# Performance work log

Measured on AMD Instinct MI355X. Metric: run time of the kernel, lower is better.

## Reference

```python
import jax, jax.numpy as jnp
import numpy as np

B, K, C, O = 8, 100000, 16, 16
HG, WG = 512, 512
ALPHA_PRIOR = 1.0
KERN = np.array([[0.075, 0.125, 0.075], [0.125, 0.3, 0.125], [0.075, 0.125, 0.075]], dtype=np.float32)


def setup_inputs() -> dict:
    key = jax.random.key(0)
    k1, k2, k3, k4, k5 = jax.random.split(key, 5)
    node_feat = jax.random.normal(k1, (B, K, C), dtype=jnp.float32)
    node_xy = jax.random.uniform(k2, (B, K, 2), dtype=jnp.float32, minval=0.0, maxval=WG - 1.0)
    node_types = jax.random.randint(k3, (B, K), 0, 2)
    # kaiming_normal_ fan_out: std = sqrt(2 / fan_out), fan_out = O*1*1
    std = (2.0 / O) ** 0.5
    w_obj = jax.random.normal(k4, (O, C), dtype=jnp.float32) * std
    w_prior = jax.random.normal(k5, (O, C), dtype=jnp.float32) * std
    hw = np.array([HG, WG], dtype=np.int64)
    return {"node_feat": node_feat, "node_xy": node_xy, "hw": hw,
            "node_types": node_types, "w_obj": w_obj, "w_prior": w_prior}


def rasterize(node_feat, node_xy, weight, H, W):
    # node_feat [B,K,C], node_xy [B,K,2], weight [B,K] 0/1 mask (masked scatter == scatter of zeros)
    xs = jnp.clip(jnp.round(node_xy[..., 0]), 0, W - 1).astype(jnp.int32)
    ys = jnp.clip(jnp.round(node_xy[..., 1]), 0, H - 1).astype(jnp.int32)
    idx = ys * W + xs  # [B,K] flat grid index
    src = node_feat * weight[..., None]  # zero out non-selected nodes

    def scat(idx_b, src_b):
        return jnp.zeros((H * W, src_b.shape[-1]), src_b.dtype).at[idx_b].add(src_b)

    grid = jax.vmap(scat)(idx, src)  # [B,HW,C]
    return grid.reshape(grid.shape[0], H, W, -1).transpose(0, 3, 1, 2)  # [B,C,H,W]


def splat3x3(x, kern):
    # depthwise 3x3 conv, groups = C
    c = x.shape[1]
    w = jnp.broadcast_to(kern[None, None], (c, 1, 3, 3))
    return jax.lax.conv_general_dilated(
        x, w, window_strides=(1, 1), padding='SAME',
        dimension_numbers=('NCHW', 'OIHW', 'NCHW'), feature_group_count=c)


def reference(node_feat, node_xy, hw, node_types, w_obj, w_prior):
    H, W = int(hw[0]), int(hw[1])
    kern = jnp.asarray(KERN)
    mask_obj = (node_types == 0).astype(node_feat.dtype)
    mask_prior = (node_types == 1).astype(node_feat.dtype)
    map_obj = splat3x3(rasterize(node_feat, node_xy, mask_obj, H, W), kern)
    map_prior = splat3x3(rasterize(node_feat, node_xy, mask_prior, H, W), kern)
    # rasterize + splat run under torch.no_grad() in the original
    map_obj = jax.lax.stop_gradient(map_obj)
    map_prior = jax.lax.stop_gradient(map_prior)
    out = jnp.einsum('oc,bchw->bohw', w_obj, map_obj) \
        + ALPHA_PRIOR * jnp.einsum('oc,bchw->bohw', w_prior, map_prior)
    return out
```

## Files before the change

kernel.cpp:

```cpp
#include <hip/hip_runtime.h>

#define B_ 8
#define K_ 100000
#define NODES (B_ * K_)
#define C_ 16
#define O_ 16
#define H_ 512
#define W_ 512
#define TSX 32
#define TSY 16
#define NTX (W_ / TSX)
#define NTY (H_ / TSY)
#define NBKT (B_ * NTX * NTY)
#define CAP 512
#define EX (TSX + 2)
#define EY (TSY + 2)
#define PLANE (EX * EY)
#define FB 1000
#define FPB (FB / B_)
#define FCHUNK (K_ / FPB)
#define IDS_OFF 16384
#define P_OFF (IDS_OFF + NBKT * CAP * 4)
#define WS_NEED ((size_t)P_OFF + (size_t)NODES * O_ * 4)

__device__ __forceinline__ float bf_lo(unsigned int u) {
    union { unsigned int i; float f; } v; v.i = u << 16; return v.f;
}
__device__ __forceinline__ float bf_hi(unsigned int u) {
    union { unsigned int i; float f; } v; v.i = u & 0xffff0000u; return v.f;
}
__device__ __forceinline__ unsigned short f2bf(float f) {
    union { float f; unsigned int u; } v; v.f = f;
    unsigned int u = v.u;
    u += 0x7fffu + ((u >> 16) & 1u);
    return (unsigned short)(u >> 16);
}

__device__ __forceinline__ int probe_fp32_ballot(const unsigned int* xy) {
    const int lane = threadIdx.x & 63;
    int bad = 0;
    #pragma unroll
    for (int k = 0; k < 4; ++k) {
        float lo = bf_lo(xy[lane + (k << 6)]);
        bad |= !(lo >= 0.0f && lo <= 512.0f);
    }
    return __ballot(bad) != 0ull;
}

__device__ __forceinline__ void decode_xy(const void* xy, int fp32, int n,
                                          int& xs, int& ys)
{
    float x, y;
    if (fp32) { float2 p = ((const float2*)xy)[n]; x = p.x; y = p.y; }
    else { unsigned int u = ((const unsigned int*)xy)[n]; x = bf_lo(u); y = bf_hi(u); }
    xs = min(max((int)rintf(x), 0), W_ - 1);
    ys = min(max((int)rintf(y), 0), H_ - 1);
}

template<bool PRE>
__global__ __launch_bounds__(256) void fill_bins(
    const void* __restrict__ feat, const void* __restrict__ xy,
    const int* __restrict__ types,
    const void* __restrict__ w_obj, const void* __restrict__ w_prior,
    int* __restrict__ cursor, int* __restrict__ ids, float* __restrict__ p)
{
    __shared__ int hist[NTX * NTY];
    __shared__ unsigned int rec[FCHUNK];
    __shared__ float wl[PRE ? 2 * O_ * C_ : 2];

    const int tid = threadIdx.x;
    const int fp32 = probe_fp32_ballot((const unsigned int*)xy);
    for (int j = tid; j < NTX * NTY; j += 256) hist[j] = 0;
    if constexpr (PRE) {
        for (int i = tid; i < 2 * O_ * C_; i += 256) {
            if (fp32) {
                wl[i] = (i < O_ * C_) ? ((const float*)w_obj)[i]
                                      : ((const float*)w_prior)[i - O_ * C_];
            } else {
                unsigned short raw = (i < O_ * C_)
                    ? ((const unsigned short*)w_obj)[i]
                    : ((const unsigned short*)w_prior)[i - O_ * C_];
                union { unsigned int u; float f; } v; v.u = ((unsigned int)raw) << 16;
                wl[i] = v.f;
            }
        }
    }
    __syncthreads();

    const int bb = blockIdx.x / FPB;
    const int local0 = (blockIdx.x % FPB) * FCHUNK;
    const int s = bb * K_ + local0;

    for (int ii = tid; ii < FCHUNK; ii += 256) {
        const int n = s + ii;
        int xs, ys; decode_xy(xy, fp32, n, xs, ys);
        const int t = (types[n] != 0);
        rec[ii] = (unsigned)(xs | (ys << 9) | (t << 18));

        if constexpr (PRE) {
            float f[16];
            if (fp32) {
                const float4* ff = (const float4*)feat + (size_t)n * 4;
                float4 a = ff[0], b2 = ff[1], c = ff[2], d = ff[3];
                f[0]=a.x; f[1]=a.y; f[2]=a.z; f[3]=a.w;
                f[4]=b2.x; f[5]=b2.y; f[6]=b2.z; f[7]=b2.w;
                f[8]=c.x; f[9]=c.y; f[10]=c.z; f[11]=c.w;
                f[12]=d.x; f[13]=d.y; f[14]=d.z; f[15]=d.w;
            } else {
                const uint4* ff = (const uint4*)feat + (size_t)n * 2;
                uint4 A = ff[0], Bv = ff[1];
                f[0]=bf_lo(A.x);  f[1]=bf_hi(A.x);  f[2]=bf_lo(A.y);  f[3]=bf_hi(A.y);
                f[4]=bf_lo(A.z);  f[5]=bf_hi(A.z);  f[6]=bf_lo(A.w);  f[7]=bf_hi(A.w);
                f[8]=bf_lo(Bv.x); f[9]=bf_hi(Bv.x); f[10]=bf_lo(Bv.y); f[11]=bf_hi(Bv.y);
                f[12]=bf_lo(Bv.z); f[13]=bf_hi(Bv.z); f[14]=bf_lo(Bv.w); f[15]=bf_hi(Bv.w);
            }
            const float* wrow = &wl[t * O_ * C_];
            float pv[16];
            #pragma unroll
            for (int o = 0; o < O_; ++o) {
                float acc = 0.f;
                #pragma unroll
                for (int c = 0; c < C_; ++c) acc = fmaf(wrow[o * C_ + c], f[c], acc);
                pv[o] = acc;
            }
            float4* pout = (float4*)(p + (size_t)n * O_);
            pout[0] = make_float4(pv[0],  pv[1],  pv[2],  pv[3]);
            pout[1] = make_float4(pv[4],  pv[5],  pv[6],  pv[7]);
            pout[2] = make_float4(pv[8],  pv[9],  pv[10], pv[11]);
            pout[3] = make_float4(pv[12], pv[13], pv[14], pv[15]);
        }

        int xlo = max((xs - 1) >> 5, 0), xhi = min((xs + 1) >> 5, NTX - 1);
        int ylo = max((ys - 1) >> 4, 0), yhi = min((ys + 1) >> 4, NTY - 1);
        for (int tyy = ylo; tyy <= yhi; ++tyy)
            for (int txx = xlo; txx <= xhi; ++txx)
                atomicAdd(&hist[tyy * NTX + txx], 1);
    }
    __syncthreads();

    for (int j = tid; j < NTX * NTY; j += 256) {
        int c = hist[j];
        hist[j] = c ? atomicAdd(&cursor[bb * NTX * NTY + j], c) : 0;
    }
    __syncthreads();

    for (int ii = tid; ii < FCHUNK; ii += 256) {
        unsigned r = rec[ii];
        int xs = r & 511, ys = (r >> 9) & 511, t = (r >> 18) & 1;
        int local = local0 + ii;
        int xlo = max((xs - 1) >> 5, 0), xhi = min((xs + 1) >> 5, NTX - 1);
        int ylo = max((ys - 1) >> 4, 0), yhi = min((ys + 1) >> 4, NTY - 1);
        for (int tyy = ylo; tyy <= yhi; ++tyy)
            for (int txx = xlo; txx <= xhi; ++txx) {
                int bk = tyy * NTX + txx;
                int slot = atomicAdd(&hist[bk], 1);
                if (slot < CAP) {
                    int lx = xs - (txx << 5) + 1;
                    int ly = ys - (tyy << 4) + 1;
                    ids[(bb * NTX * NTY + bk) * CAP + slot] =
                        local | (t << 17) | (lx << 18) | (ly << 24);
                }
            }
    }
}

template<bool PRE>
__global__ __launch_bounds__(512) void tile_fused(
    const void* __restrict__ src ,
    const void* __restrict__ xy,
    const void* __restrict__ w_obj, const void* __restrict__ w_prior,
    const int* __restrict__ cursor, const int* __restrict__ ids,
    void* __restrict__ out)
{
    __shared__ float accs[O_ * PLANE];
    __shared__ float wl[PRE ? 2 : 2 * O_ * C_];

    const int tid = threadIdx.x;
    const int tx = blockIdx.x, ty = blockIdx.y, b = blockIdx.z;
    const int bucket = (b * NTY + ty) * NTX + tx;
    int cnt = cursor[bucket];
    if (cnt > CAP) cnt = CAP;
    const int fp32 = probe_fp32_ballot((const unsigned int*)xy);

    float f[16];
    int t = 0, lx = 0, ly = 0;
    const bool active = (tid < cnt);
    if (active) {
        const unsigned pck = (unsigned)ids[bucket * CAP + tid];
        const int local = pck & 0x1FFFF;
        t  = (pck >> 17) & 1;
        lx = (pck >> 18) & 63;
        ly = (pck >> 24) & 31;
        const size_t n = (size_t)b * K_ + local;
        if constexpr (PRE) {
            const float4* pp = (const float4*)src + n * 4;
            float4 a = pp[0], b2 = pp[1], c = pp[2], d = pp[3];
            f[0]=a.x; f[1]=a.y; f[2]=a.z; f[3]=a.w;
            f[4]=b2.x; f[5]=b2.y; f[6]=b2.z; f[7]=b2.w;
            f[8]=c.x; f[9]=c.y; f[10]=c.z; f[11]=c.w;
            f[12]=d.x; f[13]=d.y; f[14]=d.z; f[15]=d.w;
        } else {
            if (fp32) {
                const float4* ff = (const float4*)src + n * 4;
                float4 a = ff[0], b2 = ff[1], c = ff[2], d = ff[3];
                f[0]=a.x; f[1]=a.y; f[2]=a.z; f[3]=a.w;
                f[4]=b2.x; f[5]=b2.y; f[6]=b2.z; f[7]=b2.w;
                f[8]=c.x; f[9]=c.y; f[10]=c.z; f[11]=c.w;
                f[12]=d.x; f[13]=d.y; f[14]=d.z; f[15]=d.w;
            } else {
                const uint4* ff = (const uint4*)src + n * 2;
                uint4 A = ff[0], Bv = ff[1];
                f[0]=bf_lo(A.x);  f[1]=bf_hi(A.x);  f[2]=bf_lo(A.y);  f[3]=bf_hi(A.y);
                f[4]=bf_lo(A.z);  f[5]=bf_hi(A.z);  f[6]=bf_lo(A.w);  f[7]=bf_hi(A.w);
                f[8]=bf_lo(Bv.x); f[9]=bf_hi(Bv.x); f[10]=bf_lo(Bv.y); f[11]=bf_hi(Bv.y);
                f[12]=bf_lo(Bv.z); f[13]=bf_hi(Bv.z); f[14]=bf_lo(Bv.w); f[15]=bf_hi(Bv.w);
            }
        }
    }

    for (int i = tid; i < O_ * PLANE; i += 512) accs[i] = 0.f;
    if constexpr (!PRE) {
        if (fp32) {
            for (int i = tid; i < 2 * O_ * C_; i += 512)
                wl[i] = (i < O_ * C_) ? ((const float*)w_obj)[i]
                                      : ((const float*)w_prior)[i - O_ * C_];
        } else {
            for (int i = tid; i < 2 * O_ * C_; i += 512) {
                unsigned short raw = (i < O_ * C_)
                    ? ((const unsigned short*)w_obj)[i]
                    : ((const unsigned short*)w_prior)[i - O_ * C_];
                union { unsigned int u; float f; } v; v.u = ((unsigned int)raw) << 16;
                wl[i] = v.f;
            }
        }
    }
    __syncthreads();

    if (active) {
        float* cell = &accs[ly * EX + lx];
        if constexpr (PRE) {
            #pragma unroll
            for (int o = 0; o < O_; ++o) atomicAdd(cell + o * PLANE, f[o]);
        } else {
            const float* wrow = &wl[t * O_ * C_];
            #pragma unroll
            for (int o = 0; o < O_; ++o) {
                float acc = 0.f;
                #pragma unroll
                for (int c = 0; c < C_; ++c) acc = fmaf(wrow[o * C_ + c], f[c], acc);
                atomicAdd(cell + o * PLANE, acc);
            }
        }
    }
    __syncthreads();

    const int x = tid & 31;
    const int o = tid >> 5;
    const float* pl = &accs[o * PLANE + x];
    float hA2 = 0.f, hA1 = 0.f, hB1 = 0.f;
    const int x0 = tx * TSX, y0 = ty * TSY;
    const size_t obase = (((size_t)(b * O_ + o)) * H_) * W_;

    #pragma unroll
    for (int iy = 0; iy < EY; ++iy) {
        float l = pl[iy * EX], c = pl[iy * EX + 1], r = pl[iy * EX + 2];
        float sfx = l + r;
        float hA = fmaf(0.075f, sfx, 0.125f * c);
        float hB = fmaf(0.125f, sfx, 0.3f * c);
        if (iy >= 2) {
            float v = hA2 + hB1 + hA;
            size_t oi = obase + (size_t)(y0 + iy - 2) * W_ + (x0 + x);
            if (fp32) __builtin_nontemporal_store(v, (float*)out + oi);
            else      __builtin_nontemporal_store(f2bf(v), (unsigned short*)out + oi);
        }
        hA2 = hA1; hA1 = hA; hB1 = hB;
    }
}

extern "C" void kernel_launch(void* const* d_in, const int* in_sizes, int n_in,
                              void* d_out, int out_size, void* d_ws, size_t ws_size,
                              hipStream_t stream)
{
    const void* feat = d_in[0];
    const void* xy = d_in[1];
    const int* types = (const int*)d_in[3];
    const void* w_obj = d_in[4];
    const void* w_prior = d_in[5];

    int* cursor = (int*)d_ws;
    int* ids = (int*)((char*)d_ws + IDS_OFF);
    float* p = (float*)((char*)d_ws + P_OFF);

    hipMemsetAsync(cursor, 0, NBKT * sizeof(int), stream);
    if (ws_size >= WS_NEED) {
        fill_bins<true><<<FB, 256, 0, stream>>>(feat, xy, types, w_obj, w_prior,
                                                cursor, ids, p);
        tile_fused<true><<<dim3(NTX, NTY, B_), 512, 0, stream>>>(
            p, xy, w_obj, w_prior, cursor, ids, d_out);
    } else {
        fill_bins<false><<<FB, 256, 0, stream>>>(feat, xy, types, w_obj, w_prior,
                                                 cursor, ids, p);
        tile_fused<false><<<dim3(NTX, NTY, B_), 512, 0, stream>>>(
            feat, xy, w_obj, w_prior, cursor, ids, d_out);
    }
}
```

Before: 285.3 us.

## Scatter projected node values directly into per-tile slots instead of index lists

Adds a new path where the fill kernel projects each node's features through the weights and writes the 16 projected values plus packed local coordinates straight into per-bucket slot storage, using global atomic cursors. The tile kernel then reads these values contiguously instead of gathering through node ids into a separate projected buffer. This removes the random indirect gather in the tile stage, at the cost of writing projected data up to four times for nodes near tile edges and needing a larger workspace. The fill grid also doubles in block count, and global atomics replace shared histograms.

```diff
diff --git a/kernel.cpp b/kernel.cpp
--- a/kernel.cpp
+++ b/kernel.cpp
@@ -16,12 +16,21 @@
 #define EX (TSX + 2)
 #define EY (TSY + 2)
 #define PLANE (EX * EY)
+
 #define FB 1000
 #define FPB (FB / B_)
 #define FCHUNK (K_ / FPB)
 #define IDS_OFF 16384
 #define P_OFF (IDS_OFF + NBKT * CAP * 4)
-#define WS_NEED ((size_t)P_OFF + (size_t)NODES * O_ * 4)
+#define WS_NEED_PRE ((size_t)P_OFF + (size_t)NODES * O_ * 4)
+
+#define SFB 2000
+#define SFPB (SFB / B_)
+#define SFCHUNK (K_ / SFPB)
+#define LXY_OFF 16384
+static inline size_t ws_need_scat(int scap) {
+    return (size_t)LXY_OFF + (size_t)NBKT * scap * 2 + (size_t)NBKT * scap * 64;
+}
 
 __device__ __forceinline__ float bf_lo(unsigned int u) {
     union { unsigned int i; float f; } v; v.i = u << 16; return v.f;
@@ -57,6 +66,164 @@
     ys = min(max((int)rintf(y), 0), H_ - 1);
 }
 
+__device__ __forceinline__ void load_feat16(const void* feat, size_t n, int fp32,
+                                            float* f)
+{
+    if (fp32) {
+        const float4* ff = (const float4*)feat + n * 4;
+        float4 a = ff[0], b2 = ff[1], c = ff[2], d = ff[3];
+        f[0]=a.x; f[1]=a.y; f[2]=a.z; f[3]=a.w;
+        f[4]=b2.x; f[5]=b2.y; f[6]=b2.z; f[7]=b2.w;
+        f[8]=c.x; f[9]=c.y; f[10]=c.z; f[11]=c.w;
+        f[12]=d.x; f[13]=d.y; f[14]=d.z; f[15]=d.w;
+    } else {
+        const uint4* ff = (const uint4*)feat + n * 2;
+        uint4 A = ff[0], Bv = ff[1];
+        f[0]=bf_lo(A.x);  f[1]=bf_hi(A.x);  f[2]=bf_lo(A.y);  f[3]=bf_hi(A.y);
+        f[4]=bf_lo(A.z);  f[5]=bf_hi(A.z);  f[6]=bf_lo(A.w);  f[7]=bf_hi(A.w);
+        f[8]=bf_lo(Bv.x); f[9]=bf_hi(Bv.x); f[10]=bf_lo(Bv.y); f[11]=bf_hi(Bv.y);
+        f[12]=bf_lo(Bv.z); f[13]=bf_hi(Bv.z); f[14]=bf_lo(Bv.w); f[15]=bf_hi(Bv.w);
+    }
+}
+
+__device__ __forceinline__ void load_weights_lds(float* wl, int fp32,
+                                                 const void* w_obj,
+                                                 const void* w_prior,
+                                                 int tid, int nthreads)
+{
+    for (int i = tid; i < 2 * O_ * C_; i += nthreads) {
+        if (fp32) {
+            wl[i] = (i < O_ * C_) ? ((const float*)w_obj)[i]
+                                  : ((const float*)w_prior)[i - O_ * C_];
+        } else {
+            unsigned short raw = (i < O_ * C_)
+                ? ((const unsigned short*)w_obj)[i]
+                : ((const unsigned short*)w_prior)[i - O_ * C_];
+            union { unsigned int u; float f; } v; v.u = ((unsigned int)raw) << 16;
+            wl[i] = v.f;
+        }
+    }
+}
+
+__global__ __launch_bounds__(256) void fill_scat(
+    const void* __restrict__ feat, const void* __restrict__ xy,
+    const int* __restrict__ types,
+    const void* __restrict__ w_obj, const void* __restrict__ w_prior,
+    int* __restrict__ cursor, float* __restrict__ slots,
+    unsigned short* __restrict__ lxy, int scap)
+{
+    __shared__ float wl[2 * O_ * C_];
+
+    const int tid = threadIdx.x;
+    const int fp32 = probe_fp32_ballot((const unsigned int*)xy);
+    load_weights_lds(wl, fp32, w_obj, w_prior, tid, 256);
+    __syncthreads();
+
+    const int bb = blockIdx.x / SFPB;
+    const int local0 = (blockIdx.x % SFPB) * SFCHUNK;
+    const int s = bb * K_ + local0;
+
+    for (int ii = tid; ii < SFCHUNK; ii += 256) {
+        const int n = s + ii;
+        int xs, ys; decode_xy(xy, fp32, n, xs, ys);
+        const int t = (types[n] != 0);
+
+        float f[16];
+        load_feat16(feat, (size_t)n, fp32, f);
+        const float* wrow = &wl[t * O_ * C_];
+        float pv[16];
+        #pragma unroll
+        for (int o = 0; o < O_; ++o) {
+            float acc = 0.f;
+            #pragma unroll
+            for (int c = 0; c < C_; ++c) acc = fmaf(wrow[o * C_ + c], f[c], acc);
+            pv[o] = acc;
+        }
+
+        const int xlo = max((xs - 1) >> 5, 0), xhi = min((xs + 1) >> 5, NTX - 1);
+        const int ylo = max((ys - 1) >> 4, 0), yhi = min((ys + 1) >> 4, NTY - 1);
+        for (int tyy = ylo; tyy <= yhi; ++tyy)
+            for (int txx = xlo; txx <= xhi; ++txx) {
+                const int bkg = (bb * NTY + tyy) * NTX + txx;
+                const int slot = atomicAdd(&cursor[bkg], 1);
+                if (slot < scap) {
+                    const size_t base = (size_t)bkg * scap + slot;
+                    float4* sp = (float4*)(slots + base * 16);
+                    sp[0] = make_float4(pv[0],  pv[1],  pv[2],  pv[3]);
+                    sp[1] = make_float4(pv[4],  pv[5],  pv[6],  pv[7]);
+                    sp[2] = make_float4(pv[8],  pv[9],  pv[10], pv[11]);
+                    sp[3] = make_float4(pv[12], pv[13], pv[14], pv[15]);
+                    const int lx = xs - (txx << 5) + 1;
+                    const int ly = ys - (tyy << 4) + 1;
+                    lxy[base] = (unsigned short)(lx | (ly << 8));
+                }
+            }
+    }
+}
+
+__global__ __launch_bounds__(512) void tile_scat(
+    const float* __restrict__ slots, const unsigned short* __restrict__ lxy,
+    const void* __restrict__ xy,
+    const int* __restrict__ cursor, void* __restrict__ out, int scap)
+{
+    __shared__ float accs[O_ * PLANE];
+
+    const int tid = threadIdx.x;
+    const int tx = blockIdx.x, ty = blockIdx.y, b = blockIdx.z;
+    const int bucket = (b * NTY + ty) * NTX + tx;
+    int cnt = cursor[bucket];
+    if (cnt > scap) cnt = scap;
+    const int fp32 = probe_fp32_ballot((const unsigned int*)xy);
+
+    float f[16];
+    int lx = 0, ly = 0;
+    const bool active = (tid < cnt);
+    if (active) {
+        const size_t base = (size_t)bucket * scap + tid;
+        const unsigned short lv = lxy[base];
+        lx = lv & 63;
+        ly = (lv >> 8) & 31;
+        const float4* sp = (const float4*)(slots + base * 16);
+        float4 a = sp[0], b2 = sp[1], c = sp[2], d = sp[3];
+        f[0]=a.x; f[1]=a.y; f[2]=a.z; f[3]=a.w;
+        f[4]=b2.x; f[5]=b2.y; f[6]=b2.z; f[7]=b2.w;
+        f[8]=c.x; f[9]=c.y; f[10]=c.z; f[11]=c.w;
+        f[12]=d.x; f[13]=d.y; f[14]=d.z; f[15]=d.w;
+    }
+
+    for (int i = tid; i < O_ * PLANE; i += 512) accs[i] = 0.f;
+    __syncthreads();
+
+    if (active) {
+        float* cell = &accs[ly * EX + lx];
+        #pragma unroll
+        for (int o = 0; o < O_; ++o) atomicAdd(cell + o * PLANE, f[o]);
+    }
+    __syncthreads();
+
+    const int x = tid & 31;
+    const int o = tid >> 5;
+    const float* pl = &accs[o * PLANE + x];
+    float hA2 = 0.f, hA1 = 0.f, hB1 = 0.f;
+    const int x0 = tx * TSX, y0 = ty * TSY;
+    const size_t obase = (((size_t)(b * O_ + o)) * H_) * W_;
+
+    #pragma unroll
+    for (int iy = 0; iy < EY; ++iy) {
+        float l = pl[iy * EX], c = pl[iy * EX + 1], r = pl[iy * EX + 2];
+        float sfx = l + r;
+        float hA = fmaf(0.075f, sfx, 0.125f * c);
+        float hB = fmaf(0.125f, sfx, 0.3f * c);
+        if (iy >= 2) {
+            float v = hA2 + hB1 + hA;
+            size_t oi = obase + (size_t)(y0 + iy - 2) * W_ + (x0 + x);
+            if (fp32) __builtin_nontemporal_store(v, (float*)out + oi);
+            else      __builtin_nontemporal_store(f2bf(v), (unsigned short*)out + oi);
+        }
+        hA2 = hA1; hA1 = hA; hB1 = hB;
+    }
+}
+
 template<bool PRE>
 __global__ __launch_bounds__(256) void fill_bins(
     const void* __restrict__ feat, const void* __restrict__ xy,
@@ -71,20 +238,7 @@
     const int tid = threadIdx.x;
     const int fp32 = probe_fp32_ballot((const unsigned int*)xy);
     for (int j = tid; j < NTX * NTY; j += 256) hist[j] = 0;
-    if constexpr (PRE) {
-        for (int i = tid; i < 2 * O_ * C_; i += 256) {
-            if (fp32) {
-                wl[i] = (i < O_ * C_) ? ((const float*)w_obj)[i]
-                                      : ((const float*)w_prior)[i - O_ * C_];
-            } else {
-                unsigned short raw = (i < O_ * C_)
-                    ? ((const unsigned short*)w_obj)[i]
-                    : ((const unsigned short*)w_prior)[i - O_ * C_];
-                union { unsigned int u; float f; } v; v.u = ((unsigned int)raw) << 16;
-                wl[i] = v.f;
-            }
-        }
-    }
+    if constexpr (PRE) load_weights_lds(wl, fp32, w_obj, w_prior, tid, 256);
     __syncthreads();
 
     const int bb = blockIdx.x / FPB;
@@ -99,21 +253,7 @@
 
         if constexpr (PRE) {
             float f[16];
-            if (fp32) {
-                const float4* ff = (const float4*)feat + (size_t)n * 4;
-                float4 a = ff[0], b2 = ff[1], c = ff[2], d = ff[3];
-                f[0]=a.x; f[1]=a.y; f[2]=a.z; f[3]=a.w;
-                f[4]=b2.x; f[5]=b2.y; f[6]=b2.z; f[7]=b2.w;
-                f[8]=c.x; f[9]=c.y; f[10]=c.z; f[11]=c.w;
-                f[12]=d.x; f[13]=d.y; f[14]=d.z; f[15]=d.w;
-            } else {
-                const uint4* ff = (const uint4*)feat + (size_t)n * 2;
-                uint4 A = ff[0], Bv = ff[1];
-                f[0]=bf_lo(A.x);  f[1]=bf_hi(A.x);  f[2]=bf_lo(A.y);  f[3]=bf_hi(A.y);
-                f[4]=bf_lo(A.z);  f[5]=bf_hi(A.z);  f[6]=bf_lo(A.w);  f[7]=bf_hi(A.w);
-                f[8]=bf_lo(Bv.x); f[9]=bf_hi(Bv.x); f[10]=bf_lo(Bv.y); f[11]=bf_hi(Bv.y);
-                f[12]=bf_lo(Bv.z); f[13]=bf_hi(Bv.z); f[14]=bf_lo(Bv.w); f[15]=bf_hi(Bv.w);
-            }
+            load_feat16(feat, (size_t)n, fp32, f);
             const float* wrow = &wl[t * O_ * C_];
             float pv[16];
             #pragma unroll
@@ -166,8 +306,7 @@
 
 template<bool PRE>
 __global__ __launch_bounds__(512) void tile_fused(
-    const void* __restrict__ src ,
-    const void* __restrict__ xy,
+    const void* __restrict__ src, const void* __restrict__ xy,
     const void* __restrict__ w_obj, const void* __restrict__ w_prior,
     const int* __restrict__ cursor, const int* __restrict__ ids,
     void* __restrict__ out)
@@ -200,40 +339,12 @@
             f[8]=c.x; f[9]=c.y; f[10]=c.z; f[11]=c.w;
             f[12]=d.x; f[13]=d.y; f[14]=d.z; f[15]=d.w;
         } else {
-            if (fp32) {
-                const float4* ff = (const float4*)src + n * 4;
-                float4 a = ff[0], b2 = ff[1], c = ff[2], d = ff[3];
-                f[0]=a.x; f[1]=a.y; f[2]=a.z; f[3]=a.w;
-                f[4]=b2.x; f[5]=b2.y; f[6]=b2.z; f[7]=b2.w;
-                f[8]=c.x; f[9]=c.y; f[10]=c.z; f[11]=c.w;
-                f[12]=d.x; f[13]=d.y; f[14]=d.z; f[15]=d.w;
-            } else {
-                const uint4* ff = (const uint4*)src + n * 2;
-                uint4 A = ff[0], Bv = ff[1];
-                f[0]=bf_lo(A.x);  f[1]=bf_hi(A.x);  f[2]=bf_lo(A.y);  f[3]=bf_hi(A.y);
-                f[4]=bf_lo(A.z);  f[5]=bf_hi(A.z);  f[6]=bf_lo(A.w);  f[7]=bf_hi(A.w);
-                f[8]=bf_lo(Bv.x); f[9]=bf_hi(Bv.x); f[10]=bf_lo(Bv.y); f[11]=bf_hi(Bv.y);
-                f[12]=bf_lo(Bv.z); f[13]=bf_hi(Bv.z); f[14]=bf_lo(Bv.w); f[15]=bf_hi(Bv.w);
-            }
+            load_feat16(src, n, fp32, f);
         }
     }
 
     for (int i = tid; i < O_ * PLANE; i += 512) accs[i] = 0.f;
-    if constexpr (!PRE) {
-        if (fp32) {
-            for (int i = tid; i < 2 * O_ * C_; i += 512)
-                wl[i] = (i < O_ * C_) ? ((const float*)w_obj)[i]
-                                      : ((const float*)w_prior)[i - O_ * C_];
-        } else {
-            for (int i = tid; i < 2 * O_ * C_; i += 512) {
-                unsigned short raw = (i < O_ * C_)
-                    ? ((const unsigned short*)w_obj)[i]
-                    : ((const unsigned short*)w_prior)[i - O_ * C_];
-                union { unsigned int u; float f; } v; v.u = ((unsigned int)raw) << 16;
-                wl[i] = v.f;
-            }
-        }
-    }
+    if constexpr (!PRE) load_weights_lds(wl, fp32, w_obj, w_prior, tid, 512);
     __syncthreads();
 
     if (active) {
@@ -288,16 +399,29 @@
     const void* w_prior = d_in[5];
 
     int* cursor = (int*)d_ws;
-    int* ids = (int*)((char*)d_ws + IDS_OFF);
-    float* p = (float*)((char*)d_ws + P_OFF);
-
     hipMemsetAsync(cursor, 0, NBKT * sizeof(int), stream);
-    if (ws_size >= WS_NEED) {
+
+    int scap = 0;
+    if (ws_size >= ws_need_scat(512)) scap = 512;
+    else if (ws_size >= ws_need_scat(384)) scap = 384;
+
+    if (scap) {
+        unsigned short* lxy = (unsigned short*)((char*)d_ws + LXY_OFF);
+        float* slots = (float*)((char*)d_ws + LXY_OFF + (size_t)NBKT * scap * 2);
+        fill_scat<<<SFB, 256, 0, stream>>>(feat, xy, types, w_obj, w_prior,
+                                           cursor, slots, lxy, scap);
+        tile_scat<<<dim3(NTX, NTY, B_), 512, 0, stream>>>(
+            slots, lxy, xy, cursor, d_out, scap);
+    } else if (ws_size >= WS_NEED_PRE) {
+        int* ids = (int*)((char*)d_ws + IDS_OFF);
+        float* p = (float*)((char*)d_ws + P_OFF);
         fill_bins<true><<<FB, 256, 0, stream>>>(feat, xy, types, w_obj, w_prior,
                                                 cursor, ids, p);
         tile_fused<true><<<dim3(NTX, NTY, B_), 512, 0, stream>>>(
             p, xy, w_obj, w_prior, cursor, ids, d_out);
     } else {
+        int* ids = (int*)((char*)d_ws + IDS_OFF);
+        float* p = (float*)((char*)d_ws + P_OFF);
         fill_bins<false><<<FB, 256, 0, stream>>>(feat, xy, types, w_obj, w_prior,
                                                  cursor, ids, p);
         tile_fused<false><<<dim3(NTX, NTY, B_), 512, 0, stream>>>(
```

New measurement: 375.5 us. 1.32x slower.
